# Kernel optimization log

Measured on AMD Instinct MI355X. Metric: run time of the kernel, lower is better.

## Reference

```python
import jax, jax.numpy as jnp
import numpy as np

N, E, IN, HID, OUT = 100000, 1600000, 128, 64, 64
NEG = 0.2   # GATConv negative_slope default
EPS = 1e-5


def _gat(x, src, dst, W, a_s, a_d, b, n):
    # PyG GATConv, heads=1: h = x W; e_ij = LeakyReLU(a_s.h_j + a_d.h_i);
    # softmax over incoming edges of i; out_i = sum_j alpha_ij h_j + b
    h = x @ W                                   # [N, F]
    s = (h @ a_s)[src] + (h @ a_d)[dst]         # [E]
    e = jnp.where(s >= 0, s, NEG * s)
    m = jax.ops.segment_max(e, dst, num_segments=n)
    w = jnp.exp(e - m[dst])
    z = jax.ops.segment_sum(w, dst, num_segments=n)
    alpha = w / z[dst]
    out = jax.ops.segment_sum(h[src] * alpha[:, None], dst, num_segments=n)
    return out + b


def _graph_ln(x, g, b):
    # PyG LayerNorm mode='graph' (default): normalize over all nodes+features
    mu = jnp.mean(x)
    var = jnp.mean((x - mu) ** 2)
    return (x - mu) * jax.lax.rsqrt(var + EPS) * g + b


def _prelu(x, a):
    return jnp.where(x >= 0, x, a * x)


def _encoder(x, edge_index, params):
    n = x.shape[0]
    loops = jnp.arange(n, dtype=edge_index.dtype)  # GATConv add_self_loops=True
    src = jnp.concatenate([edge_index[0], loops])
    dst = jnp.concatenate([edge_index[1], loops])
    for (W, a_s, a_d, b, g, be, p) in params:
        x = _gat(x, src, dst, W, a_s, a_d, b, n)
        x = _graph_ln(x, g, be)
        x = _prelu(x, p)
    return x


def setup_inputs():
    key = jax.random.key(0)
    ks = jax.random.split(key, 32)
    d = {}
    d["x_q"] = jax.random.normal(ks[0], (N, IN), jnp.float32)
    d["x_k"] = jax.random.normal(ks[1], (N, IN), jnp.float32)
    d["edge_index_q"] = jax.random.randint(ks[2], (2, E), 0, N)
    d["edge_index_k"] = jax.random.randint(ks[3], (2, E), 0, N)
    i = 4
    for pre, fi, fo in [("q1", IN, HID), ("q2", HID, OUT), ("k1", IN, HID), ("k2", HID, OUT)]:
        d[pre + "_W"] = jax.random.normal(ks[i], (fi, fo), jnp.float32) / np.sqrt(fi).astype(np.float32); i += 1
        d[pre + "_as"] = jax.random.normal(ks[i], (fo,), jnp.float32) * 0.1; i += 1
        d[pre + "_ad"] = jax.random.normal(ks[i], (fo,), jnp.float32) * 0.1; i += 1
        d[pre + "_b"] = jnp.zeros((fo,), jnp.float32)
        d[pre + "_g"] = jnp.ones((fo,), jnp.float32)
        d[pre + "_be"] = jnp.zeros((fo,), jnp.float32)
        d[pre + "_p"] = jnp.full((1,), 0.25, jnp.float32)
    d["m_W1"] = jax.random.normal(ks[i], (OUT, 2 * OUT), jnp.float32) / np.sqrt(OUT).astype(np.float32); i += 1
    d["m_b1"] = jnp.zeros((2 * OUT,), jnp.float32)
    d["m_p"] = jnp.full((1,), 0.25, jnp.float32)
    d["m_W2"] = jax.random.normal(ks[i], (2 * OUT, OUT), jnp.float32) / np.sqrt(2 * OUT).astype(np.float32)
    d["m_b2"] = jnp.zeros((OUT,), jnp.float32)
    return d


def reference(x_q, x_k, edge_index_q, edge_index_k,
              q1_W, q1_as, q1_ad, q1_b, q1_g, q1_be, q1_p,
              q2_W, q2_as, q2_ad, q2_b, q2_g, q2_be, q2_p,
              k1_W, k1_as, k1_ad, k1_b, k1_g, k1_be, k1_p,
              k2_W, k2_as, k2_ad, k2_b, k2_g, k2_be, k2_p,
              m_W1, m_b1, m_p, m_W2, m_b2):
    Q = _encoder(x_q, edge_index_q,
                 [(q1_W, q1_as, q1_ad, q1_b, q1_g, q1_be, q1_p),
                  (q2_W, q2_as, q2_ad, q2_b, q2_g, q2_be, q2_p)])
    Q = _prelu(Q @ m_W1 + m_b1, m_p) @ m_W2 + m_b2
    K = _encoder(x_k, edge_index_k,
                 [(k1_W, k1_as, k1_ad, k1_b, k1_g, k1_be, k1_p),
                  (k2_W, k2_as, k2_ad, k2_b, k2_g, k2_be, k2_p)])
    return (Q, jax.lax.stop_gradient(K))
```

## Files before the change

kernel.cpp:

```cpp
#include <hip/hip_runtime.h>
#include <cstddef>
#include <cstdint>

#define NEG_SLOPE 0.2f
#define LN_EPS    1e-5f
#define NBUK      256
#define MAXNPB    512

typedef unsigned short ushort_t;
typedef short bf16x8 __attribute__((ext_vector_type(8)));
typedef float f32x4  __attribute__((ext_vector_type(4)));

__device__ __forceinline__ float lrelu(float s) { return s >= 0.f ? s : NEG_SLOPE * s; }
__device__ __forceinline__ float b2f(ushort_t u) { return __uint_as_float(((uint32_t)u) << 16); }
__device__ __forceinline__ ushort_t f2b(float f) {
  uint32_t u = __float_as_uint(f);
  return (ushort_t)((u + 0x7fffu + ((u >> 16) & 1u)) >> 16);
}
__device__ __forceinline__ uint2 pack4(float4 v) {
  uint2 r;
  r.x = (uint32_t)f2b(v.x) | ((uint32_t)f2b(v.y) << 16);
  r.y = (uint32_t)f2b(v.z) | ((uint32_t)f2b(v.w) << 16);
  return r;
}

__global__ __launch_bounds__(256) void kb_count(const int* __restrict__ dst, int E,
                                                int* __restrict__ gbcnt, uint32_t bmul) {
  __shared__ int hist[NBUK];
  const int tid = threadIdx.x;
  hist[tid] = 0;
  __syncthreads();
  int i = blockIdx.x * blockDim.x + tid;
  const int stride = gridDim.x * blockDim.x;
  for (; i < E; i += stride) atomicAdd(&hist[__umulhi((uint32_t)dst[i], bmul)], 1);
  __syncthreads();
  atomicAdd(&gbcnt[tid], hist[tid]);
}

__global__ __launch_bounds__(256) void kb_scan(const int* __restrict__ gbcnt,
                                               int* __restrict__ boff, int* __restrict__ gbcur,
                                               int* __restrict__ nlo,
                                               uint32_t bmul, int N, int E) {
  __shared__ int ps[NBUK];
  const int t = threadIdx.x;
  const int v = gbcnt[t];
  ps[t] = v;
  __syncthreads();
  for (int off = 1; off < NBUK; off <<= 1) {
    const int x = (t >= off) ? ps[t - off] : 0;
    __syncthreads();
    ps[t] += x;
    __syncthreads();
  }
  const int excl = ps[t] - v;
  boff[t] = excl;
  gbcur[t] = excl;
  if (t == NBUK - 1) boff[NBUK] = E;
  uint64_t lo = ((uint64_t)t << 32) + (uint64_t)bmul - 1;
  int nl = (int)(lo / (uint64_t)bmul);
  nlo[t] = nl < N ? nl : N;
  if (t == NBUK - 1) nlo[NBUK] = N;
}

__global__ __launch_bounds__(256) void kb_expand(const int* __restrict__ src,
                                                 const int* __restrict__ dst, int E,
                                                 int* __restrict__ gbcur,
                                                 int2* __restrict__ pairs, uint32_t bmul) {
  __shared__ int hist[NBUK], base[NBUK], lcnt[NBUK];
  const int tid = threadIdx.x;
  const int nchunk = (E + 4095) >> 12;
  for (int c = blockIdx.x; c < nchunk; c += gridDim.x) {
    const int e0 = c << 12;
    hist[tid] = 0; lcnt[tid] = 0;
    __syncthreads();
    int sv[16], dv[16], bv[16];
    #pragma unroll
    for (int u = 0; u < 16; ++u) {
      const int i = e0 + u * 256 + tid;
      if (i < E) {
        sv[u] = src[i]; dv[u] = dst[i];
        bv[u] = (int)__umulhi((uint32_t)dv[u], bmul);
        atomicAdd(&hist[bv[u]], 1);
      } else bv[u] = -1;
    }
    __syncthreads();
    base[tid] = atomicAdd(&gbcur[tid], hist[tid]);
    __syncthreads();
    #pragma unroll
    for (int u = 0; u < 16; ++u) {
      if (bv[u] >= 0) {
        const int pos = atomicAdd(&lcnt[bv[u]], 1);
        pairs[base[bv[u]] + pos] = make_int2(sv[u], dv[u]);
      }
    }
    __syncthreads();
  }
}

__global__ __launch_bounds__(256) void kb_sort(const int2* __restrict__ pairs,
                                               const int* __restrict__ boff,
                                               const int* __restrict__ nlo,
                                               int* __restrict__ rowp, int* __restrict__ csr,
                                               int N, int E) {
  __shared__ int hist[MAXNPB];
  __shared__ int ps[256];
  const int b = blockIdx.x, tid = threadIdx.x;
  const int n0 = nlo[b], nn = nlo[b + 1] - n0;
  const int e0 = boff[b], e1 = boff[b + 1];
  for (int k = tid; k < nn; k += 256) hist[k] = 0;
  __syncthreads();
  for (int i = e0 + tid; i < e1; i += 256) atomicAdd(&hist[pairs[i].y - n0], 1);
  __syncthreads();
  const int i0 = 2 * tid, i1 = 2 * tid + 1;
  const int a = (i0 < nn) ? hist[i0] : 0;
  const int c = (i1 < nn) ? hist[i1] : 0;
  const int tot = a + c;
  ps[tid] = tot;
  __syncthreads();
  for (int off = 1; off < 256; off <<= 1) {
    const int x = (tid >= off) ? ps[tid - off] : 0;
    __syncthreads();
    ps[tid] += x;
    __syncthreads();
  }
  const int excl = ps[tid] - tot;
  if (i0 < nn) { hist[i0] = excl;     rowp[n0 + i0] = e0 + excl; }
  if (i1 < nn) { hist[i1] = excl + a; rowp[n0 + i1] = e0 + excl + a; }
  if (b == gridDim.x - 1 && tid == 0) rowp[N] = E;
  __syncthreads();
  for (int i = e0 + tid; i < e1; i += 256) {
    const int2 e = pairs[i];
    const int p = atomicAdd(&hist[e.y - n0], 1);
    csr[e0 + p] = e.x;
  }
}

template <int FI, bool LNF>
__global__ __launch_bounds__(256) void k_gemm_att(
    const float* __restrict__ act, int N,
    const float* __restrict__ W, const float* __restrict__ a_s, const float* __restrict__ a_d,
    const float* __restrict__ stats, const float* __restrict__ g,
    const float* __restrict__ be, const float* __restrict__ pp,
    ushort_t* __restrict__ h16, float* __restrict__ hs, float* __restrict__ hd)
{
  constexpr int P = FI + 8;
  __shared__ ushort_t S[64 * P];
  const int tid = threadIdx.x, wid = tid >> 6, lane = tid & 63;
  const int l15 = lane & 15, lhi = lane >> 4;

  for (int idx = tid; idx < FI * 64; idx += 256) {
    const int k = idx >> 6, f = idx & 63;
    S[f * P + k] = f2b(W[idx]);
  }
  __syncthreads();
  bf16x8 Bf[FI / 32][4];
  #pragma unroll
  for (int kt = 0; kt < FI / 32; ++kt)
    #pragma unroll
    for (int nt = 0; nt < 4; ++nt)
      Bf[kt][nt] = *(const bf16x8*)&S[(nt * 16 + l15) * P + kt * 32 + lhi * 8];
  __syncthreads();

  float asf[4], adf[4];
  #pragma unroll
  for (int nt = 0; nt < 4; ++nt) { asf[nt] = a_s[nt * 16 + l15]; adf[nt] = a_d[nt * 16 + l15]; }
  float mu = 0.f, rstd = 1.f, p0 = 0.f;
  if (LNF) { mu = stats[0]; rstd = stats[1]; p0 = pp[0]; }

  const int ntiles = (N + 63) >> 6;
  for (int tile = blockIdx.x; tile < ntiles; tile += gridDim.x) {
    const int nb = tile << 6;
    {
      const int r = tid >> 2;
      const int node = nb + r;
      if (node < N) {
        const float4* src = (const float4*)(act + (size_t)node * FI);
        #pragma unroll
        for (int i = 0; i < FI / 16; ++i) {
          const int c = (tid & 3) * (FI / 4) + i * 4;
          float4 v = src[c >> 2];
          if (LNF) {
            const float4 gg = ((const float4*)g)[c >> 2];
            const float4 bb = ((const float4*)be)[c >> 2];
            v.x = (v.x - mu) * rstd * gg.x + bb.x;  v.x = v.x >= 0.f ? v.x : p0 * v.x;
            v.y = (v.y - mu) * rstd * gg.y + bb.y;  v.y = v.y >= 0.f ? v.y : p0 * v.y;
            v.z = (v.z - mu) * rstd * gg.z + bb.z;  v.z = v.z >= 0.f ? v.z : p0 * v.z;
            v.w = (v.w - mu) * rstd * gg.w + bb.w;  v.w = v.w >= 0.f ? v.w : p0 * v.w;
          }
          *(uint2*)&S[r * P + c] = pack4(v);
        }
      }
    }
    __syncthreads();

    const f32x4 fz = {0.f, 0.f, 0.f, 0.f};
    f32x4 acc[4]; acc[0] = fz; acc[1] = fz; acc[2] = fz; acc[3] = fz;
    #pragma unroll
    for (int kt = 0; kt < FI / 32; ++kt) {
      const bf16x8 Af = *(const bf16x8*)&S[(wid * 16 + l15) * P + kt * 32 + lhi * 8];
      #pragma unroll
      for (int nt = 0; nt < 4; ++nt)
        acc[nt] = __builtin_amdgcn_mfma_f32_16x16x32_bf16(Af, Bf[kt][nt], acc[nt], 0, 0, 0);
    }
    #pragma unroll
    for (int r = 0; r < 4; ++r) {
      float ps = acc[0][r] * asf[0] + acc[1][r] * asf[1] + acc[2][r] * asf[2] + acc[3][r] * asf[3];
      float pd = acc[0][r] * adf[0] + acc[1][r] * adf[1] + acc[2][r] * adf[2] + acc[3][r] * adf[3];
      #pragma unroll
      for (int off = 1; off < 16; off <<= 1) { ps += __shfl_xor(ps, off); pd += __shfl_xor(pd, off); }
      const int node = nb + wid * 16 + lhi * 4 + r;
      if (l15 == 0 && node < N) { hs[node] = ps; hd[node] = pd; }
    }
    #pragma unroll
    for (int nt = 0; nt < 4; ++nt)
      #pragma unroll
      for (int r = 0; r < 4; ++r)
        S[(wid * 16 + lhi * 4 + r) * P + nt * 16 + l15] = f2b(acc[nt][r]);
    __syncthreads();
    {
      const int r = tid >> 2, chunk = tid & 3;
      const int node = nb + r;
      if (node < N) {
        const int4* sp = (const int4*)&S[r * P + chunk * 16];
        const int4 v0 = sp[0], v1 = sp[1];
        int4* dp = (int4*)(h16 + (size_t)node * 64 + chunk * 16);
        dp[0] = v0; dp[1] = v1;
      }
    }
    __syncthreads();
  }
}

__global__ __launch_bounds__(256) void k_aggregate(
    const int* __restrict__ rowp, const int* __restrict__ csr,
    const ushort_t* __restrict__ h16, const float* __restrict__ hs, const float* __restrict__ hd,
    const float* __restrict__ bias, int N,
    float* __restrict__ y, float* __restrict__ part)
{
  __shared__ float wsh[4][32];
  __shared__ float sh1[4], sh2[4];
  const int tid = threadIdx.x, wid = tid >> 6, lane = tid & 63;
  const int node = blockIdx.x * 4 + wid;
  float val = 0.f;
  if (node < N) {
    const float hdi = hd[node];
    const float wself = __expf(lrelu(hs[node] + hdi));
    float z = wself;
    float acc0 = wself * b2f(h16[((size_t)(uint32_t)node << 6) + lane]);
    float acc1 = 0.f, acc2 = 0.f, acc3 = 0.f;
    const int st = __builtin_amdgcn_readfirstlane(rowp[node]);
    const int en = __builtin_amdgcn_readfirstlane(rowp[node + 1]);
    for (int j = st; j < en; j += 32) {
      const int m = min(32, en - j);
      int sA = 0;
      if (lane < m) sA = csr[j + lane];
      #define GA(u) h16[((size_t)(uint32_t)__builtin_amdgcn_readlane(sA, u) << 6) + lane]
      ushort_t g0 = 0, g1 = 0, g2 = 0, g3 = 0, g4 = 0, g5 = 0, g6 = 0, g7 = 0;
      ushort_t g8 = 0, g9 = 0, g10 = 0, g11 = 0, g12 = 0, g13 = 0, g14 = 0, g15 = 0;
      ushort_t g16 = 0, g17 = 0, g18 = 0, g19 = 0, g20 = 0, g21 = 0, g22 = 0, g23 = 0;
      ushort_t g24 = 0, g25 = 0, g26 = 0, g27 = 0, g28 = 0, g29 = 0, g30 = 0, g31 = 0;
      if (m > 0)  { g0  = GA(0);  g1  = GA(1);  g2  = GA(2);  g3  = GA(3);  }
      if (m > 4)  { g4  = GA(4);  g5  = GA(5);  g6  = GA(6);  g7  = GA(7);  }
      if (m > 8)  { g8  = GA(8);  g9  = GA(9);  g10 = GA(10); g11 = GA(11); }
      if (m > 12) { g12 = GA(12); g13 = GA(13); g14 = GA(14); g15 = GA(15); }
      if (m > 16) { g16 = GA(16); g17 = GA(17); g18 = GA(18); g19 = GA(19); }
      if (m > 20) { g20 = GA(20); g21 = GA(21); g22 = GA(22); g23 = GA(23); }
      if (m > 24) { g24 = GA(24); g25 = GA(25); g26 = GA(26); g27 = GA(27); }
      if (m > 28) { g28 = GA(28); g29 = GA(29); g30 = GA(30); g31 = GA(31); }
      #undef GA
      float wA = 0.f;
      if (lane < m) wA = __expf(lrelu(hs[sA] + hdi));
      if (lane < 32) wsh[wid][lane] = wA;
      float ws = wA;
      #pragma unroll
      for (int off = 32; off; off >>= 1) ws += __shfl_xor(ws, off);
      z += ws;
      #define CS(u, a) a = fmaf(wsh[wid][u], b2f(g##u), a)
      if (m > 0)  { CS(0, acc0);  CS(1, acc1);  CS(2, acc2);  CS(3, acc3);  }
      if (m > 4)  { CS(4, acc0);  CS(5, acc1);  CS(6, acc2);  CS(7, acc3);  }
      if (m > 8)  { CS(8, acc0);  CS(9, acc1);  CS(10, acc2); CS(11, acc3); }
      if (m > 12) { CS(12, acc0); CS(13, acc1); CS(14, acc2); CS(15, acc3); }
      if (m > 16) { CS(16, acc0); CS(17, acc1); CS(18, acc2); CS(19, acc3); }
      if (m > 20) { CS(20, acc0); CS(21, acc1); CS(22, acc2); CS(23, acc3); }
      if (m > 24) { CS(24, acc0); CS(25, acc1); CS(26, acc2); CS(27, acc3); }
      if (m > 28) { CS(28, acc0); CS(29, acc1); CS(30, acc2); CS(31, acc3); }
      #undef CS
    }
    val = ((acc0 + acc1) + (acc2 + acc3)) / z + bias[lane];
    y[(size_t)node * 64 + lane] = val;
  }
  float s1r = val, s2r = val * val;
  #pragma unroll
  for (int off = 32; off; off >>= 1) { s1r += __shfl_xor(s1r, off); s2r += __shfl_xor(s2r, off); }
  if (lane == 0) { sh1[wid] = s1r; sh2[wid] = s2r; }
  __syncthreads();
  if (tid == 0) {
    part[(size_t)blockIdx.x * 2 + 0] = sh1[0] + sh1[1] + sh1[2] + sh1[3];
    part[(size_t)blockIdx.x * 2 + 1] = sh2[0] + sh2[1] + sh2[2] + sh2[3];
  }
}

__global__ __launch_bounds__(1024) void k_ln_stats(
    const float* __restrict__ part, int nblk, float invCount, float* __restrict__ statsOut)
{
  __shared__ float sh1[16], sh2[16];
  float s1 = 0.f, s2 = 0.f;
  for (int i = threadIdx.x; i < nblk; i += 1024) { s1 += part[(size_t)i * 2]; s2 += part[(size_t)i * 2 + 1]; }
  #pragma unroll
  for (int off = 32; off; off >>= 1) { s1 += __shfl_xor(s1, off); s2 += __shfl_xor(s2, off); }
  const int wid = threadIdx.x >> 6, lane = threadIdx.x & 63;
  if (lane == 0) { sh1[wid] = s1; sh2[wid] = s2; }
  __syncthreads();
  if (threadIdx.x == 0) {
    float t1 = 0.f, t2 = 0.f;
    #pragma unroll
    for (int i = 0; i < 16; ++i) { t1 += sh1[i]; t2 += sh2[i]; }
    const float mu = t1 * invCount;
    const float var = t2 * invCount - mu * mu;
    statsOut[0] = mu;
    statsOut[1] = rsqrtf(var + LN_EPS);
  }
}

__global__ __launch_bounds__(256) void k_mlp(
    const float* __restrict__ y, int N,
    const float* __restrict__ stats, const float* __restrict__ g,
    const float* __restrict__ be, const float* __restrict__ pe,
    const float* __restrict__ W1, const float* __restrict__ b1, const float* __restrict__ pm,
    const float* __restrict__ W2, const float* __restrict__ b2,
    float* __restrict__ outp)
{
  __shared__ ushort_t W1t[128 * 72];
  __shared__ ushort_t W2t[64 * 136];
  __shared__ ushort_t At[64 * 72];
  __shared__ ushort_t Tt[64 * 136];
  __shared__ float    Ob[64 * 68];
  const int tid = threadIdx.x, wid = tid >> 6, lane = tid & 63;
  const int l15 = lane & 15, lhi = lane >> 4;

  for (int idx = tid; idx < 64 * 128; idx += 256) {
    const int k = idx >> 7, f = idx & 127;
    W1t[f * 72 + k] = f2b(W1[idx]);
  }
  for (int idx = tid; idx < 128 * 64; idx += 256) {
    const int k = idx >> 6, f = idx & 63;
    W2t[f * 136 + k] = f2b(W2[idx]);
  }
  __syncthreads();

  const float mu = stats[0], rstd = stats[1], p0 = pe[0], pm0 = pm[0];
  float b1f[8], b2f_[4];
  #pragma unroll
  for (int nt = 0; nt < 8; ++nt) b1f[nt] = b1[nt * 16 + l15];
  #pragma unroll
  for (int nt = 0; nt < 4; ++nt) b2f_[nt] = b2[nt * 16 + l15];

  const int ntiles = (N + 63) >> 6;
  for (int tile = blockIdx.x; tile < ntiles; tile += gridDim.x) {
    const int nb = tile << 6;
    {
      const int r = tid >> 2;
      const int node = nb + r;
      if (node < N) {
        const float4* src = (const float4*)(y + (size_t)node * 64);
        #pragma unroll
        for (int i = 0; i < 4; ++i) {
          const int c = (tid & 3) * 16 + i * 4;
          float4 v = src[c >> 2];
          const float4 gg = ((const float4*)g)[c >> 2];
          const float4 bb = ((const float4*)be)[c >> 2];
          v.x = (v.x - mu) * rstd * gg.x + bb.x;  v.x = v.x >= 0.f ? v.x : p0 * v.x;
          v.y = (v.y - mu) * rstd * gg.y + bb.y;  v.y = v.y >= 0.f ? v.y : p0 * v.y;
          v.z = (v.z - mu) * rstd * gg.z + bb.z;  v.z = v.z >= 0.f ? v.z : p0 * v.z;
          v.w = (v.w - mu) * rstd * gg.w + bb.w;  v.w = v.w >= 0.f ? v.w : p0 * v.w;
          *(uint2*)&At[r * 72 + c] = pack4(v);
        }
      }
    }
    __syncthreads();

    const f32x4 fz = {0.f, 0.f, 0.f, 0.f};
    f32x4 acc1[8];
    #pragma unroll
    for (int nt = 0; nt < 8; ++nt) acc1[nt] = fz;
    #pragma unroll
    for (int kt = 0; kt < 2; ++kt) {
      const bf16x8 Af = *(const bf16x8*)&At[(wid * 16 + l15) * 72 + kt * 32 + lhi * 8];
      #pragma unroll
      for (int nt = 0; nt < 8; ++nt) {
        const bf16x8 Bf = *(const bf16x8*)&W1t[(nt * 16 + l15) * 72 + kt * 32 + lhi * 8];
        acc1[nt] = __builtin_amdgcn_mfma_f32_16x16x32_bf16(Af, Bf, acc1[nt], 0, 0, 0);
      }
    }
    #pragma unroll
    for (int nt = 0; nt < 8; ++nt)
      #pragma unroll
      for (int r = 0; r < 4; ++r) {
        float v = acc1[nt][r] + b1f[nt];
        v = v >= 0.f ? v : pm0 * v;
        Tt[(wid * 16 + lhi * 4 + r) * 136 + nt * 16 + l15] = f2b(v);
      }
    __syncthreads();

    f32x4 acc2[4];
    #pragma unroll
    for (int nt = 0; nt < 4; ++nt) acc2[nt] = fz;
    #pragma unroll
    for (int kt = 0; kt < 4; ++kt) {
      const bf16x8 Af = *(const bf16x8*)&Tt[(wid * 16 + l15) * 136 + kt * 32 + lhi * 8];
      #pragma unroll
      for (int nt = 0; nt < 4; ++nt) {
        const bf16x8 Bf = *(const bf16x8*)&W2t[(nt * 16 + l15) * 136 + kt * 32 + lhi * 8];
        acc2[nt] = __builtin_amdgcn_mfma_f32_16x16x32_bf16(Af, Bf, acc2[nt], 0, 0, 0);
      }
    }
    #pragma unroll
    for (int nt = 0; nt < 4; ++nt)
      #pragma unroll
      for (int r = 0; r < 4; ++r)
        Ob[(wid * 16 + lhi * 4 + r) * 68 + nt * 16 + l15] = acc2[nt][r] + b2f_[nt];
    __syncthreads();
    {
      const int r = tid >> 2, chunk = tid & 3;
      const int node = nb + r;
      if (node < N) {
        const float4* sp = (const float4*)&Ob[r * 68 + chunk * 16];
        const float4 v0 = sp[0], v1 = sp[1], v2 = sp[2], v3 = sp[3];
        float4* dp = (float4*)(outp + (size_t)node * 64 + chunk * 16);
        dp[0] = v0; dp[1] = v1; dp[2] = v2; dp[3] = v3;
      }
    }
    __syncthreads();
  }
}

__global__ void k_ln_prelu_out(const float4* __restrict__ y4, int total4,
                               const float* __restrict__ stats, const float* __restrict__ g,
                               const float* __restrict__ be, const float* __restrict__ pe,
                               float4* __restrict__ o4)
{
  const float mu = stats[0], rstd = stats[1], p0 = pe[0];
  int i = blockIdx.x * blockDim.x + threadIdx.x;
  const int stride = gridDim.x * blockDim.x;
  for (; i < total4; i += stride) {
    const int f = (i & 15) << 2;
    float4 v = y4[i];
    const float4 gg = *(const float4*)(g + f);
    const float4 bb = *(const float4*)(be + f);
    v.x = (v.x - mu) * rstd * gg.x + bb.x;  v.x = v.x >= 0.f ? v.x : p0 * v.x;
    v.y = (v.y - mu) * rstd * gg.y + bb.y;  v.y = v.y >= 0.f ? v.y : p0 * v.y;
    v.z = (v.z - mu) * rstd * gg.z + bb.z;  v.z = v.z >= 0.f ? v.z : p0 * v.z;
    v.w = (v.w - mu) * rstd * gg.w + bb.w;  v.w = v.w >= 0.f ? v.w : p0 * v.w;
    o4[i] = v;
  }
}

extern "C" void kernel_launch(void* const* d_in, const int* in_sizes, int n_in,
                              void* d_out, int out_size, void* d_ws, size_t ws_size,
                              hipStream_t stream) {
  (void)n_in; (void)out_size; (void)ws_size;
  const int FIN = 128, F = 64;
  const int N = in_sizes[0] / FIN;
  const int E = in_sizes[2] / 2;

  const float* x_q = (const float*)d_in[0];
  const float* x_k = (const float*)d_in[1];
  const int*   ei_q = (const int*)d_in[2];
  const int*   ei_k = (const int*)d_in[3];
  const float* L[4][7];
  for (int l = 0; l < 4; ++l)
    for (int j = 0; j < 7; ++j) L[l][j] = (const float*)d_in[4 + l * 7 + j];
  const float* mW1 = (const float*)d_in[32];
  const float* mb1 = (const float*)d_in[33];
  const float* mp  = (const float*)d_in[34];
  const float* mW2 = (const float*)d_in[35];
  const float* mb2 = (const float*)d_in[36];
  float* out = (float*)d_out;

  char* w = (char*)d_ws;
  auto alloc = [&](size_t bytes) { char* r = w; w += (bytes + 255) & ~size_t(255); return r; };
  ushort_t* h16 = (ushort_t*)alloc((size_t)N * F * sizeof(ushort_t));
  float* yb    = (float*)alloc((size_t)N * F * sizeof(float));
  float* hs    = (float*)alloc((size_t)N * sizeof(float));
  float* hd    = (float*)alloc((size_t)N * sizeof(float));
  const int nblk = (N + 3) / 4;
  float* part  = (float*)alloc((size_t)nblk * 2 * sizeof(float));
  float* stats = (float*)alloc(16 * sizeof(float));
  int* rowp    = (int*)alloc((size_t)(N + 1) * sizeof(int));
  int* csr     = (int*)alloc((size_t)E * sizeof(int));
  int* bcnt    = (int*)alloc(NBUK * sizeof(int));
  int* boff    = (int*)alloc((NBUK + 1) * sizeof(int));
  int* bcur    = (int*)alloc(NBUK * sizeof(int));
  int* nlo     = (int*)alloc((NBUK + 1) * sizeof(int));
  int2* pairs  = (int2*)yb;

  const float invCount = 1.f / ((float)N * (float)F);
  const uint32_t bmul = (uint32_t)(((uint64_t)NBUK << 32) / (uint64_t)N);

  auto build_csr = [&](const int* ei) {
    hipMemsetAsync(bcnt, 0, NBUK * sizeof(int), stream);
    kb_count<<<512, 256, 0, stream>>>(ei + E, E, bcnt, bmul);
    kb_scan<<<1, NBUK, 0, stream>>>(bcnt, boff, bcur, nlo, bmul, N, E);
    kb_expand<<<512, 256, 0, stream>>>(ei, ei + E, E, bcur, pairs, bmul);
    kb_sort<<<NBUK, 256, 0, stream>>>(pairs, boff, nlo, rowp, csr, N, E);
  };

  auto run_layers = [&](const float* x0, int li0) {
    const float* const* A = L[li0];
    k_gemm_att<128, false><<<512, 256, 0, stream>>>(
        x0, N, A[0], A[1], A[2], nullptr, nullptr, nullptr, nullptr, h16, hs, hd);
    k_aggregate<<<nblk, 256, 0, stream>>>(rowp, csr, h16, hs, hd, A[3], N, yb, part);
    k_ln_stats<<<1, 1024, 0, stream>>>(part, nblk, invCount, stats + 2 * li0);
    const float* const* B = L[li0 + 1];
    k_gemm_att<64, true><<<512, 256, 0, stream>>>(
        yb, N, B[0], B[1], B[2], stats + 2 * li0, A[4], A[5], A[6], h16, hs, hd);
    k_aggregate<<<nblk, 256, 0, stream>>>(rowp, csr, h16, hs, hd, B[3], N, yb, part);
    k_ln_stats<<<1, 1024, 0, stream>>>(part, nblk, invCount, stats + 2 * (li0 + 1));
  };

  build_csr(ei_q);
  run_layers(x_q, 0);
  k_mlp<<<512, 256, 0, stream>>>(yb, N, stats + 2, L[1][4], L[1][5], L[1][6],
                                 mW1, mb1, mp, mW2, mb2, out);

  build_csr(ei_k);
  run_layers(x_k, 2);
  const int total4 = N * F / 4;
  k_ln_prelu_out<<<2048, 256, 0, stream>>>((const float4*)yb, total4, stats + 6,
                                           L[3][4], L[3][5], L[3][6],
                                           (float4*)(out + (size_t)N * F));
}
```

Measured before the change: 487.8 us.

## Drop CSR count pass with fixed-capacity buckets and store activations as bf16

The CSR build no longer counts and scans bucket sizes. Each bucket gets a fixed capacity of 1.5x the mean edge count, and per-node start and end arrays replace rowptr, which removes the count kernel, the scan kernel and a memset per encoder. The aggregate output is now stored as bf16 instead of fp32, halving its traffic in the GEMM, MLP and output kernels. The risks are overflow when a bucket exceeds its capacity (edges are silently dropped through the min clamp) and extra rounding error from the bf16 intermediate.

```diff
diff --git a/kernel.cpp b/kernel.cpp
--- a/kernel.cpp
+++ b/kernel.cpp
@@ -24,42 +24,9 @@
   return r;
 }
 
-__global__ __launch_bounds__(256) void kb_count(const int* __restrict__ dst, int E,
-                                                int* __restrict__ gbcnt, uint32_t bmul) {
-  __shared__ int hist[NBUK];
-  const int tid = threadIdx.x;
-  hist[tid] = 0;
-  __syncthreads();
-  int i = blockIdx.x * blockDim.x + tid;
-  const int stride = gridDim.x * blockDim.x;
-  for (; i < E; i += stride) atomicAdd(&hist[__umulhi((uint32_t)dst[i], bmul)], 1);
-  __syncthreads();
-  atomicAdd(&gbcnt[tid], hist[tid]);
-}
-
-__global__ __launch_bounds__(256) void kb_scan(const int* __restrict__ gbcnt,
-                                               int* __restrict__ boff, int* __restrict__ gbcur,
-                                               int* __restrict__ nlo,
-                                               uint32_t bmul, int N, int E) {
-  __shared__ int ps[NBUK];
-  const int t = threadIdx.x;
-  const int v = gbcnt[t];
-  ps[t] = v;
-  __syncthreads();
-  for (int off = 1; off < NBUK; off <<= 1) {
-    const int x = (t >= off) ? ps[t - off] : 0;
-    __syncthreads();
-    ps[t] += x;
-    __syncthreads();
-  }
-  const int excl = ps[t] - v;
-  boff[t] = excl;
-  gbcur[t] = excl;
-  if (t == NBUK - 1) boff[NBUK] = E;
-  uint64_t lo = ((uint64_t)t << 32) + (uint64_t)bmul - 1;
-  int nl = (int)(lo / (uint64_t)bmul);
-  nlo[t] = nl < N ? nl : N;
-  if (t == NBUK - 1) nlo[NBUK] = N;
+
+__global__ void kb_init(int* __restrict__ gbcur, int cap) {
+  gbcur[threadIdx.x] = threadIdx.x * cap;
 }
 
 __global__ __launch_bounds__(256) void kb_expand(const int* __restrict__ src,
@@ -98,15 +65,20 @@
 }
 
 __global__ __launch_bounds__(256) void kb_sort(const int2* __restrict__ pairs,
-                                               const int* __restrict__ boff,
-                                               const int* __restrict__ nlo,
-                                               int* __restrict__ rowp, int* __restrict__ csr,
-                                               int N, int E) {
+                                               const int* __restrict__ gbcur,
+                                               int* __restrict__ rs, int* __restrict__ re,
+                                               int* __restrict__ csr,
+                                               uint32_t bmul, int cap, int N) {
   __shared__ int hist[MAXNPB];
   __shared__ int ps[256];
   const int b = blockIdx.x, tid = threadIdx.x;
-  const int n0 = nlo[b], nn = nlo[b + 1] - n0;
-  const int e0 = boff[b], e1 = boff[b + 1];
+  int n0 = (int)((((uint64_t)b << 32) + bmul - 1) / bmul);
+  int n1 = (int)((((uint64_t)(b + 1) << 32) + bmul - 1) / bmul);
+  n0 = n0 < N ? n0 : N;
+  n1 = n1 < N ? n1 : N;
+  const int nn = n1 - n0;
+  const int e0 = b * cap;
+  const int e1 = min(gbcur[b], e0 + cap);
   for (int k = tid; k < nn; k += 256) hist[k] = 0;
   __syncthreads();
   for (int i = e0 + tid; i < e1; i += 256) atomicAdd(&hist[pairs[i].y - n0], 1);
@@ -124,9 +96,8 @@
     __syncthreads();
   }
   const int excl = ps[tid] - tot;
-  if (i0 < nn) { hist[i0] = excl;     rowp[n0 + i0] = e0 + excl; }
-  if (i1 < nn) { hist[i1] = excl + a; rowp[n0 + i1] = e0 + excl + a; }
-  if (b == gridDim.x - 1 && tid == 0) rowp[N] = E;
+  if (i0 < nn) { hist[i0] = excl;     rs[n0 + i0] = e0 + excl;     re[n0 + i0] = e0 + excl + a; }
+  if (i1 < nn) { hist[i1] = excl + a; rs[n0 + i1] = e0 + excl + a; re[n0 + i1] = e0 + excl + a + c; }
   __syncthreads();
   for (int i = e0 + tid; i < e1; i += 256) {
     const int2 e = pairs[i];
@@ -137,7 +108,7 @@
 
 template <int FI, bool LNF>
 __global__ __launch_bounds__(256) void k_gemm_att(
-    const float* __restrict__ act, int N,
+    const void* __restrict__ act, int N,
     const float* __restrict__ W, const float* __restrict__ a_s, const float* __restrict__ a_d,
     const float* __restrict__ stats, const float* __restrict__ g,
     const float* __restrict__ be, const float* __restrict__ pp,
@@ -174,20 +145,36 @@
       const int r = tid >> 2;
       const int node = nb + r;
       if (node < N) {
-        const float4* src = (const float4*)(act + (size_t)node * FI);
-        #pragma unroll
-        for (int i = 0; i < FI / 16; ++i) {
-          const int c = (tid & 3) * (FI / 4) + i * 4;
-          float4 v = src[c >> 2];
-          if (LNF) {
-            const float4 gg = ((const float4*)g)[c >> 2];
-            const float4 bb = ((const float4*)be)[c >> 2];
-            v.x = (v.x - mu) * rstd * gg.x + bb.x;  v.x = v.x >= 0.f ? v.x : p0 * v.x;
-            v.y = (v.y - mu) * rstd * gg.y + bb.y;  v.y = v.y >= 0.f ? v.y : p0 * v.y;
-            v.z = (v.z - mu) * rstd * gg.z + bb.z;  v.z = v.z >= 0.f ? v.z : p0 * v.z;
-            v.w = (v.w - mu) * rstd * gg.w + bb.w;  v.w = v.w >= 0.f ? v.w : p0 * v.w;
+        if (LNF) {
+          const ushort_t* a16 = (const ushort_t*)act;
+          const int q = tid & 3;
+          const int4* srcp = (const int4*)(a16 + (size_t)node * 64 + q * 16);
+          const int4 A0 = srcp[0], A1 = srcp[1];
+          const ushort_t* pu0 = (const ushort_t*)&A0;
+          const ushort_t* pu1 = (const ushort_t*)&A1;
+          float vv[16];
+          #pragma unroll
+          for (int i = 0; i < 8; ++i) { vv[i] = b2f(pu0[i]); vv[8 + i] = b2f(pu1[i]); }
+          #pragma unroll
+          for (int i2 = 0; i2 < 4; ++i2) {
+            const int c4 = q * 4 + i2;
+            const float4 gg = ((const float4*)g)[c4];
+            const float4 bb = ((const float4*)be)[c4];
+            float4 v;
+            v.x = (vv[i2 * 4 + 0] - mu) * rstd * gg.x + bb.x;  v.x = v.x >= 0.f ? v.x : p0 * v.x;
+            v.y = (vv[i2 * 4 + 1] - mu) * rstd * gg.y + bb.y;  v.y = v.y >= 0.f ? v.y : p0 * v.y;
+            v.z = (vv[i2 * 4 + 2] - mu) * rstd * gg.z + bb.z;  v.z = v.z >= 0.f ? v.z : p0 * v.z;
+            v.w = (vv[i2 * 4 + 3] - mu) * rstd * gg.w + bb.w;  v.w = v.w >= 0.f ? v.w : p0 * v.w;
+            *(uint2*)&S[r * P + c4 * 4] = pack4(v);
           }
-          *(uint2*)&S[r * P + c] = pack4(v);
+        } else {
+          const float4* srcp = (const float4*)((const float*)act + (size_t)node * FI);
+          #pragma unroll
+          for (int i = 0; i < FI / 16; ++i) {
+            const int c = (tid & 3) * (FI / 4) + i * 4;
+            const float4 v = srcp[c >> 2];
+            *(uint2*)&S[r * P + c] = pack4(v);
+          }
         }
       }
     }
@@ -232,10 +219,10 @@
 }
 
 __global__ __launch_bounds__(256) void k_aggregate(
-    const int* __restrict__ rowp, const int* __restrict__ csr,
+    const int* __restrict__ rs, const int* __restrict__ re, const int* __restrict__ csr,
     const ushort_t* __restrict__ h16, const float* __restrict__ hs, const float* __restrict__ hd,
     const float* __restrict__ bias, int N,
-    float* __restrict__ y, float* __restrict__ part)
+    ushort_t* __restrict__ y16, float* __restrict__ part)
 {
   __shared__ float wsh[4][32];
   __shared__ float sh1[4], sh2[4];
@@ -248,8 +235,8 @@
     float z = wself;
     float acc0 = wself * b2f(h16[((size_t)(uint32_t)node << 6) + lane]);
     float acc1 = 0.f, acc2 = 0.f, acc3 = 0.f;
-    const int st = __builtin_amdgcn_readfirstlane(rowp[node]);
-    const int en = __builtin_amdgcn_readfirstlane(rowp[node + 1]);
+    const int st = __builtin_amdgcn_readfirstlane(rs[node]);
+    const int en = __builtin_amdgcn_readfirstlane(re[node]);
     for (int j = st; j < en; j += 32) {
       const int m = min(32, en - j);
       int sA = 0;
@@ -287,7 +274,7 @@
       #undef CS
     }
     val = ((acc0 + acc1) + (acc2 + acc3)) / z + bias[lane];
-    y[(size_t)node * 64 + lane] = val;
+    y16[(size_t)node * 64 + lane] = f2b(val);
   }
   float s1r = val, s2r = val * val;
   #pragma unroll
@@ -323,7 +310,7 @@
 }
 
 __global__ __launch_bounds__(256) void k_mlp(
-    const float* __restrict__ y, int N,
+    const ushort_t* __restrict__ y16, int N,
     const float* __restrict__ stats, const float* __restrict__ g,
     const float* __restrict__ be, const float* __restrict__ pe,
     const float* __restrict__ W1, const float* __restrict__ b1, const float* __restrict__ pm,
@@ -362,18 +349,25 @@
       const int r = tid >> 2;
       const int node = nb + r;
       if (node < N) {
-        const float4* src = (const float4*)(y + (size_t)node * 64);
+        const int q = tid & 3;
+        const int4* srcp = (const int4*)(y16 + (size_t)node * 64 + q * 16);
+        const int4 A0 = srcp[0], A1 = srcp[1];
+        const ushort_t* pu0 = (const ushort_t*)&A0;
+        const ushort_t* pu1 = (const ushort_t*)&A1;
+        float vv[16];
         #pragma unroll
-        for (int i = 0; i < 4; ++i) {
-          const int c = (tid & 3) * 16 + i * 4;
-          float4 v = src[c >> 2];
-          const float4 gg = ((const float4*)g)[c >> 2];
-          const float4 bb = ((const float4*)be)[c >> 2];
-          v.x = (v.x - mu) * rstd * gg.x + bb.x;  v.x = v.x >= 0.f ? v.x : p0 * v.x;
-          v.y = (v.y - mu) * rstd * gg.y + bb.y;  v.y = v.y >= 0.f ? v.y : p0 * v.y;
-          v.z = (v.z - mu) * rstd * gg.z + bb.z;  v.z = v.z >= 0.f ? v.z : p0 * v.z;
-          v.w = (v.w - mu) * rstd * gg.w + bb.w;  v.w = v.w >= 0.f ? v.w : p0 * v.w;
-          *(uint2*)&At[r * 72 + c] = pack4(v);
+        for (int i = 0; i < 8; ++i) { vv[i] = b2f(pu0[i]); vv[8 + i] = b2f(pu1[i]); }
+        #pragma unroll
+        for (int i2 = 0; i2 < 4; ++i2) {
+          const int c4 = q * 4 + i2;
+          const float4 gg = ((const float4*)g)[c4];
+          const float4 bb = ((const float4*)be)[c4];
+          float4 v;
+          v.x = (vv[i2 * 4 + 0] - mu) * rstd * gg.x + bb.x;  v.x = v.x >= 0.f ? v.x : p0 * v.x;
+          v.y = (vv[i2 * 4 + 1] - mu) * rstd * gg.y + bb.y;  v.y = v.y >= 0.f ? v.y : p0 * v.y;
+          v.z = (vv[i2 * 4 + 2] - mu) * rstd * gg.z + bb.z;  v.z = v.z >= 0.f ? v.z : p0 * v.z;
+          v.w = (vv[i2 * 4 + 3] - mu) * rstd * gg.w + bb.w;  v.w = v.w >= 0.f ? v.w : p0 * v.w;
+          *(uint2*)&At[r * 72 + c4 * 4] = pack4(v);
         }
       }
     }
@@ -434,24 +428,31 @@
   }
 }
 
-__global__ void k_ln_prelu_out(const float4* __restrict__ y4, int total4,
+__global__ void k_ln_prelu_out(const ushort_t* __restrict__ y16, int total8,
                                const float* __restrict__ stats, const float* __restrict__ g,
                                const float* __restrict__ be, const float* __restrict__ pe,
-                               float4* __restrict__ o4)
+                               float* __restrict__ o)
 {
   const float mu = stats[0], rstd = stats[1], p0 = pe[0];
   int i = blockIdx.x * blockDim.x + threadIdx.x;
   const int stride = gridDim.x * blockDim.x;
-  for (; i < total4; i += stride) {
-    const int f = (i & 15) << 2;
-    float4 v = y4[i];
-    const float4 gg = *(const float4*)(g + f);
-    const float4 bb = *(const float4*)(be + f);
-    v.x = (v.x - mu) * rstd * gg.x + bb.x;  v.x = v.x >= 0.f ? v.x : p0 * v.x;
-    v.y = (v.y - mu) * rstd * gg.y + bb.y;  v.y = v.y >= 0.f ? v.y : p0 * v.y;
-    v.z = (v.z - mu) * rstd * gg.z + bb.z;  v.z = v.z >= 0.f ? v.z : p0 * v.z;
-    v.w = (v.w - mu) * rstd * gg.w + bb.w;  v.w = v.w >= 0.f ? v.w : p0 * v.w;
-    o4[i] = v;
+  for (; i < total8; i += stride) {
+    const int4 A = *(const int4*)(y16 + (size_t)i * 8);
+    const ushort_t* pu = (const ushort_t*)&A;
+    const int grp = i & 7;
+    const float4 g0 = ((const float4*)g)[grp * 2], g1 = ((const float4*)g)[grp * 2 + 1];
+    const float4 b0 = ((const float4*)be)[grp * 2], b1 = ((const float4*)be)[grp * 2 + 1];
+    float4 o0, o1;
+    o0.x = (b2f(pu[0]) - mu) * rstd * g0.x + b0.x;  o0.x = o0.x >= 0.f ? o0.x : p0 * o0.x;
+    o0.y = (b2f(pu[1]) - mu) * rstd * g0.y + b0.y;  o0.y = o0.y >= 0.f ? o0.y : p0 * o0.y;
+    o0.z = (b2f(pu[2]) - mu) * rstd * g0.z + b0.z;  o0.z = o0.z >= 0.f ? o0.z : p0 * o0.z;
+    o0.w = (b2f(pu[3]) - mu) * rstd * g0.w + b0.w;  o0.w = o0.w >= 0.f ? o0.w : p0 * o0.w;
+    o1.x = (b2f(pu[4]) - mu) * rstd * g1.x + b1.x;  o1.x = o1.x >= 0.f ? o1.x : p0 * o1.x;
+    o1.y = (b2f(pu[5]) - mu) * rstd * g1.y + b1.y;  o1.y = o1.y >= 0.f ? o1.y : p0 * o1.y;
+    o1.z = (b2f(pu[6]) - mu) * rstd * g1.z + b1.z;  o1.z = o1.z >= 0.f ? o1.z : p0 * o1.z;
+    o1.w = (b2f(pu[7]) - mu) * rstd * g1.w + b1.w;  o1.w = o1.w >= 0.f ? o1.w : p0 * o1.w;
+    float4* dp = (float4*)(o + (size_t)i * 8);
+    dp[0] = o0; dp[1] = o1;
   }
 }
 
@@ -477,56 +478,54 @@
   const float* mb2 = (const float*)d_in[36];
   float* out = (float*)d_out;
 
+  const int CAP = (((E + NBUK - 1) / NBUK) * 3 / 2 + 3) & ~3;
+
   char* w = (char*)d_ws;
   auto alloc = [&](size_t bytes) { char* r = w; w += (bytes + 255) & ~size_t(255); return r; };
   ushort_t* h16 = (ushort_t*)alloc((size_t)N * F * sizeof(ushort_t));
-  float* yb    = (float*)alloc((size_t)N * F * sizeof(float));
+  ushort_t* y16 = (ushort_t*)alloc((size_t)N * F * sizeof(ushort_t));
   float* hs    = (float*)alloc((size_t)N * sizeof(float));
   float* hd    = (float*)alloc((size_t)N * sizeof(float));
   const int nblk = (N + 3) / 4;
   float* part  = (float*)alloc((size_t)nblk * 2 * sizeof(float));
   float* stats = (float*)alloc(16 * sizeof(float));
-  int* rowp    = (int*)alloc((size_t)(N + 1) * sizeof(int));
-  int* csr     = (int*)alloc((size_t)E * sizeof(int));
-  int* bcnt    = (int*)alloc(NBUK * sizeof(int));
-  int* boff    = (int*)alloc((NBUK + 1) * sizeof(int));
+  int* rs      = (int*)alloc((size_t)N * sizeof(int));
+  int* re      = (int*)alloc((size_t)N * sizeof(int));
+  int* csr     = (int*)alloc((size_t)NBUK * CAP * sizeof(int));
   int* bcur    = (int*)alloc(NBUK * sizeof(int));
-  int* nlo     = (int*)alloc((NBUK + 1) * sizeof(int));
-  int2* pairs  = (int2*)yb;
+  int2* pairs  = (int2*)alloc((size_t)NBUK * CAP * sizeof(int2));
 
   const float invCount = 1.f / ((float)N * (float)F);
   const uint32_t bmul = (uint32_t)(((uint64_t)NBUK << 32) / (uint64_t)N);
 
   auto build_csr = [&](const int* ei) {
-    hipMemsetAsync(bcnt, 0, NBUK * sizeof(int), stream);
-    kb_count<<<512, 256, 0, stream>>>(ei + E, E, bcnt, bmul);
-    kb_scan<<<1, NBUK, 0, stream>>>(bcnt, boff, bcur, nlo, bmul, N, E);
+    kb_init<<<1, NBUK, 0, stream>>>(bcur, CAP);
     kb_expand<<<512, 256, 0, stream>>>(ei, ei + E, E, bcur, pairs, bmul);
-    kb_sort<<<NBUK, 256, 0, stream>>>(pairs, boff, nlo, rowp, csr, N, E);
+    kb_sort<<<NBUK, 256, 0, stream>>>(pairs, bcur, rs, re, csr, bmul, CAP, N);
   };
 
   auto run_layers = [&](const float* x0, int li0) {
     const float* const* A = L[li0];
     k_gemm_att<128, false><<<512, 256, 0, stream>>>(
         x0, N, A[0], A[1], A[2], nullptr, nullptr, nullptr, nullptr, h16, hs, hd);
-    k_aggregate<<<nblk, 256, 0, stream>>>(rowp, csr, h16, hs, hd, A[3], N, yb, part);
+    k_aggregate<<<nblk, 256, 0, stream>>>(rs, re, csr, h16, hs, hd, A[3], N, y16, part);
     k_ln_stats<<<1, 1024, 0, stream>>>(part, nblk, invCount, stats + 2 * li0);
     const float* const* B = L[li0 + 1];
     k_gemm_att<64, true><<<512, 256, 0, stream>>>(
-        yb, N, B[0], B[1], B[2], stats + 2 * li0, A[4], A[5], A[6], h16, hs, hd);
-    k_aggregate<<<nblk, 256, 0, stream>>>(rowp, csr, h16, hs, hd, B[3], N, yb, part);
+        y16, N, B[0], B[1], B[2], stats + 2 * li0, A[4], A[5], A[6], h16, hs, hd);
+    k_aggregate<<<nblk, 256, 0, stream>>>(rs, re, csr, h16, hs, hd, B[3], N, y16, part);
     k_ln_stats<<<1, 1024, 0, stream>>>(part, nblk, invCount, stats + 2 * (li0 + 1));
   };
 
   build_csr(ei_q);
   run_layers(x_q, 0);
-  k_mlp<<<512, 256, 0, stream>>>(yb, N, stats + 2, L[1][4], L[1][5], L[1][6],
+  k_mlp<<<512, 256, 0, stream>>>(y16, N, stats + 2, L[1][4], L[1][5], L[1][6],
                                  mW1, mb1, mp, mW2, mb2, out);
 
   build_csr(ei_k);
   run_layers(x_k, 2);
-  const int total4 = N * F / 4;
-  k_ln_prelu_out<<<2048, 256, 0, stream>>>((const float4*)yb, total4, stats + 6,
+  const int total8 = N * F / 8;
+  k_ln_prelu_out<<<2048, 256, 0, stream>>>(y16, total8, stats + 6,
                                            L[3][4], L[3][5], L[3][6],
-                                           (float4*)(out + (size_t)N * F));
-}
+                                           out + (size_t)N * F);
+}
```

New measurement: 453.7 us. -7.0%, faster.
